# Optimization experiments

Hardware: AMD Instinct MI355X
Metric: run time of the kernel (lower is better)

The kernel has to match this reference:

```python
import jax, jax.numpy as jnp
import numpy as np

D_MODEL, N_HEADS, D_C, D_COMP, D_ROPE = 2048, 16, 512, 768, 64
D_HEAD = D_MODEL // N_HEADS  # 128
B, S = 2, 2048
ROPE_THETA = 10000.0


def _rope_cos_sin(seq_len, dim):
    # frequencies for pairwise complex rotation, dim = per-head rope dim (even)
    inv_freq = 1.0 / (ROPE_THETA ** (jnp.arange(0, dim, 2, dtype=jnp.float32) / dim))
    t = jnp.arange(seq_len, dtype=jnp.float32)
    ang = t[:, None] * inv_freq[None, :]  # [S, dim/2]
    return jnp.cos(ang), jnp.sin(ang)


def _apply_rope(x, cos, sin):
    # x: [B, S, H, dr]; rotate consecutive pairs (view_as_complex semantics)
    x1, x2 = x[..., 0::2], x[..., 1::2]
    c = cos[None, :, None, :]
    s = sin[None, :, None, :]
    y1 = x1 * c - x2 * s
    y2 = x1 * s + x2 * c
    return jnp.stack([y1, y2], axis=-1).reshape(x.shape)


def setup_inputs() -> dict:
    key = jax.random.key(0)
    ks = jax.random.split(key, 9)
    sc = 0.02
    return {
        "x": jax.random.normal(ks[0], (B, S, D_MODEL), jnp.float32),
        "Wd": jax.random.normal(ks[1], (D_MODEL, D_C), jnp.float32) * sc,
        "bd": jnp.zeros((D_C,), jnp.float32),
        "Wu": jax.random.normal(ks[2], (D_C, N_HEADS * D_HEAD), jnp.float32) * sc,
        "bu": jnp.zeros((N_HEADS * D_HEAD,), jnp.float32),
        "Wqd": jax.random.normal(ks[3], (D_MODEL, D_COMP), jnp.float32) * sc,
        "bqd": jnp.zeros((D_COMP,), jnp.float32),
        "Wqu": jax.random.normal(ks[4], (D_COMP, N_HEADS * D_HEAD), jnp.float32) * sc,
        "bqu": jnp.zeros((N_HEADS * D_HEAD,), jnp.float32),
        "Wqr": jax.random.normal(ks[5], (D_COMP, N_HEADS * D_ROPE), jnp.float32) * sc,
        "bqr": jnp.zeros((N_HEADS * D_ROPE,), jnp.float32),
        "Wkr": jax.random.normal(ks[6], (D_MODEL, N_HEADS * D_ROPE), jnp.float32) * sc,
        "bkr": jnp.zeros((N_HEADS * D_ROPE,), jnp.float32),
        "Wo": jax.random.normal(ks[7], (N_HEADS * D_HEAD, D_MODEL), jnp.float32) * sc,
        "bo": jnp.zeros((D_MODEL,), jnp.float32),
    }


def reference(x, Wd, bd, Wu, bu, Wqd, bqd, Wqu, bqu, Wqr, bqr, Wkr, bkr, Wo, bo):
    b, s, _ = x.shape
    # low-rank KV compression
    kv_c = x @ Wd + bd                                   # [B,S,d_c]
    kv_up = (kv_c @ Wu + bu).reshape(b, s, N_HEADS, D_HEAD)  # shared K-content / V
    # low-rank Q compression
    q_cmp = x @ Wqd + bqd                                # [B,S,d_comp]
    q_c = (q_cmp @ Wqu + bqu).reshape(b, s, N_HEADS, D_HEAD)
    # decoupled RoPE branches
    cos, sin = _rope_cos_sin(s, D_ROPE)
    q_r = _apply_rope((q_cmp @ Wqr + bqr).reshape(b, s, N_HEADS, D_ROPE), cos, sin)
    k_r = _apply_rope((x @ Wkr + bkr).reshape(b, s, N_HEADS, D_ROPE), cos, sin)
    q = jnp.concatenate([q_c, q_r], axis=-1)             # [B,S,H,dh+dr]
    k = jnp.concatenate([kv_up, k_r], axis=-1)           # [B,S,H,dh+dr]
    scale = 1.0 / np.sqrt(D_HEAD).astype(np.float32)
    scores = jnp.einsum('bqhd,bkhd->bhqk', q, k) * scale  # [B,H,S,S]
    probs = jax.nn.softmax(scores, axis=-1)
    out = jnp.einsum('bhqk,bkhd->bqhd', probs, kv_up)    # v == kv_up (as in source)
    out = out.reshape(b, s, N_HEADS * D_HEAD)
    return out @ Wo + bo
```

## Files before the change

kernel.cpp:

```cpp
#include <hip/hip_runtime.h>
#include <cmath>

typedef __bf16 bf16;
typedef __bf16 bf16x8 __attribute__((ext_vector_type(8)));
typedef __bf16 bf16x4 __attribute__((ext_vector_type(4)));
typedef __bf16 bf16x2 __attribute__((ext_vector_type(2)));
typedef float f32x4 __attribute__((ext_vector_type(4)));
typedef float f32x16 __attribute__((ext_vector_type(16)));
typedef int i32x4 __attribute__((ext_vector_type(4)));
typedef int i32x2 __attribute__((ext_vector_type(2)));

#define S_LEN 2048
#define QK_LD 3072

__device__ __forceinline__ void async_copy16(const bf16* g, bf16* l) {
    __builtin_amdgcn_global_load_lds(
        (const __attribute__((address_space(1))) void*)g,
        (__attribute__((address_space(3))) void*)l, 16, 0, 0);
}

__device__ __forceinline__ unsigned packbf(float a, float b) {
    bf16x2 v; v[0] = (bf16)a; v[1] = (bf16)b;
    return __builtin_bit_cast(unsigned, v);
}

__global__ __launch_bounds__(256) void cast_f32_bf16(const float* __restrict__ in,
                                                     bf16* __restrict__ out) {
    size_t i = ((size_t)blockIdx.x * 256 + threadIdx.x) * 8;
    float4 a = *(const float4*)(in + i);
    float4 b = *(const float4*)(in + i + 4);
    bf16x8 v;
    v[0] = (bf16)a.x; v[1] = (bf16)a.y; v[2] = (bf16)a.z; v[3] = (bf16)a.w;
    v[4] = (bf16)b.x; v[5] = (bf16)b.y; v[6] = (bf16)b.z; v[7] = (bf16)b.w;
    *(bf16x8*)(out + i) = v;
}

struct TSeg { const float* src; bf16* dst; int K, N, blk0; };
struct TArgs { TSeg s[7]; };

__global__ __launch_bounds__(256) void transpose_all(TArgs a) {
    __shared__ float tile[64][68];
    int b = blockIdx.x, si = 0;
#pragma unroll
    for (int i = 1; i < 7; ++i) if (b >= a.s[i].blk0) si = i;
    TSeg sg = a.s[si];
    int local = b - sg.blk0;
    int kTiles = sg.K >> 6;
    int kt = local % kTiles, nt = local / kTiles;
    int k0 = kt * 64, n0 = nt * 64;
    int K = sg.K, N = sg.N;
    int t = threadIdx.x;
#pragma unroll
    for (int i = 0; i < 4; ++i) {
        int c = t + i * 256;
        int r = c >> 4, off = (c & 15) * 4;
        float4 v = *(const float4*)(sg.src + (size_t)(k0 + r) * N + n0 + off);
        tile[r][off] = v.x; tile[r][off + 1] = v.y;
        tile[r][off + 2] = v.z; tile[r][off + 3] = v.w;
    }
    __syncthreads();
#pragma unroll
    for (int i = 0; i < 2; ++i) {
        int c = t + i * 256;
        int nr = c >> 3, koff = (c & 7) * 8;
        bf16x8 v;
#pragma unroll
        for (int j = 0; j < 8; ++j) v[j] = (bf16)tile[koff + j][nr];
        *(bf16x8*)(sg.dst + (size_t)(n0 + nr) * K + k0 + koff) = v;
    }
}

__global__ __launch_bounds__(256) void setup_small(const float* __restrict__ bd,
                                                   const float* __restrict__ bqd,
                                                   const float* __restrict__ bkr,
                                                   const float* __restrict__ bqu,
                                                   const float* __restrict__ bqr,
                                                   float* __restrict__ bcat,
                                                   float2* __restrict__ tab) {
    if (blockIdx.x < 21) {
        int i = blockIdx.x * 256 + threadIdx.x;
        if (i < 512) bcat[i] = bd[i];
        else if (i < 1280) bcat[i] = bqd[i - 512];
        else if (i < 2304) bcat[i] = bkr[i - 1280];
        else if (i < 4352) bcat[i] = bqu[i - 2304];
        else if (i < 5376) bcat[i] = bqr[i - 4352];
    } else {
        int id = (blockIdx.x - 21) * 256 + threadIdx.x;
        int s = id >> 5, i = id & 31;
        float f = expf(-0.2878231366242557f * (float)i);
        float ang = (float)s * f;
        tab[id] = make_float2(cosf(ang), sinf(ang));
    }
}

__device__ __forceinline__ void gemm_core(const bf16* __restrict__ A, int lda,
                                          const bf16* __restrict__ Bt,
                                          const float* __restrict__ bias,
                                          void* __restrict__ out0,
                                          void* __restrict__ out1,
                                          int Ndim, int Kdim, int mode,
                                          const float2* __restrict__ tab,
                                          int bn, int bm, bf16* As, bf16* Bs) {
    int t = threadIdx.x;
    int w = t >> 6, lane = t & 63;
    int wm = (w >> 1) * 64, wn = (w & 1) * 64;
    int l15 = lane & 15, q4 = lane >> 4;
    f32x4 acc[4][4] = {};

    int lrow = lane >> 2;
    int lcol = (lane & 3) * 8;
    int c0 = w * 2, c1 = w * 2 + 1;
    const bf16* aS0 = A  + (size_t)(bm * 128 + c0 * 16 + lrow) * lda + lcol;
    const bf16* aS1 = A  + (size_t)(bm * 128 + c1 * 16 + lrow) * lda + lcol;
    const bf16* bS0 = Bt + (size_t)(bn * 128 + c0 * 16 + lrow) * Kdim + lcol;
    const bf16* bS1 = Bt + (size_t)(bn * 128 + c1 * 16 + lrow) * Kdim + lcol;
    bf16* aD0 = &As[c0 * 512]; bf16* aD1 = &As[c1 * 512];
    bf16* bD0 = &Bs[c0 * 512]; bf16* bD1 = &Bs[c1 * 512];

    for (int kt = 0; kt < Kdim; kt += 32) {
        async_copy16(aS0 + kt, aD0);
        async_copy16(aS1 + kt, aD1);
        async_copy16(bS0 + kt, bD0);
        async_copy16(bS1 + kt, bD1);
        __syncthreads();
        bf16x8 af[4], bfr[4];
#pragma unroll
        for (int mb = 0; mb < 4; ++mb)
            af[mb] = *(const bf16x8*)&As[(wm + mb * 16 + l15) * 32 + q4 * 8];
#pragma unroll
        for (int nb = 0; nb < 4; ++nb)
            bfr[nb] = *(const bf16x8*)&Bs[(wn + nb * 16 + l15) * 32 + q4 * 8];
#pragma unroll
        for (int mb = 0; mb < 4; ++mb)
#pragma unroll
            for (int nb = 0; nb < 4; ++nb)
                acc[mb][nb] = __builtin_amdgcn_mfma_f32_16x16x32_bf16(
                    af[mb], bfr[nb], acc[mb][nb], 0, 0, 0);
        __syncthreads();
    }

#pragma unroll
    for (int mb = 0; mb < 4; ++mb) {
        int row = bm * 128 + wm + mb * 16 + q4 * 4;
#pragma unroll
        for (int nb = 0; nb < 4; ++nb) {
            int col = bn * 128 + wn + nb * 16 + l15;
            float bv = bias[col];
            if (mode == 1) {
#pragma unroll
                for (int r = 0; r < 4; ++r)
                    ((float*)out0)[(size_t)(row + r) * Ndim + col] = acc[mb][nb][r] + bv;
            } else if (mode == 4) {
                if (col < 1280) {
#pragma unroll
                    for (int r = 0; r < 4; ++r)
                        ((bf16*)out0)[(size_t)(row + r) * 2304 + col] =
                            (bf16)(acc[mb][nb][r] + bv);
                } else {
                    int rel = col - 1280;
                    int hh = rel >> 6, idx = rel & 63, ii = idx >> 1, odd = idx & 1;
#pragma unroll
                    for (int r = 0; r < 4; ++r) {
                        float vv = acc[mb][nb][r] + bv;
                        float pp = __shfl_xor(vv, 1, 64);
                        float2 cs = tab[((row + r) & 2047) * 32 + ii];
                        float o = vv * cs.x + (odd ? pp * cs.y : -pp * cs.y);
                        ((bf16*)out1)[(size_t)(row + r) * QK_LD + hh * 192 + 128 + idx] =
                            (bf16)o;
                    }
                }
            } else if (mode == 5) {
                if (col < 2048) {
                    int hh = col >> 7, dd = col & 127;
#pragma unroll
                    for (int r = 0; r < 4; ++r)
                        ((bf16*)out0)[(size_t)(row + r) * QK_LD + hh * 192 + dd] =
                            (bf16)(acc[mb][nb][r] + bv);
                } else {
                    int rel = col - 2048;
                    int hh = rel >> 6, idx = rel & 63, ii = idx >> 1, odd = idx & 1;
#pragma unroll
                    for (int r = 0; r < 4; ++r) {
                        float vv = acc[mb][nb][r] + bv;
                        float pp = __shfl_xor(vv, 1, 64);
                        float2 cs = tab[((row + r) & 2047) * 32 + ii];
                        float o = vv * cs.x + (odd ? pp * cs.y : -pp * cs.y);
                        ((bf16*)out0)[(size_t)(row + r) * QK_LD + hh * 192 + 128 + idx] =
                            (bf16)o;
                    }
                }
            } else {
                int hh = col >> 7, dd = col & 127;
                bf16x4 pack;
#pragma unroll
                for (int r = 0; r < 4; ++r) {
                    float vv = acc[mb][nb][r] + bv;
                    ((bf16*)out0)[(size_t)(row + r) * QK_LD + hh * 192 + dd] = (bf16)vv;
                    pack[r] = (bf16)vv;
                }
                int bidx = row >> 11, srow = row & 2047;
                *(bf16x4*)((bf16*)out1 +
                           ((size_t)(bidx * 16 + hh) * 128 + dd) * S_LEN + srow) = pack;
            }
        }
    }
}

__global__ __launch_bounds__(256) void gemm_bt(const bf16* __restrict__ A, int lda,
                                               const bf16* __restrict__ Bt,
                                               const float* __restrict__ bias,
                                               void* __restrict__ out0,
                                               void* __restrict__ out1,
                                               int Ndim, int Kdim, int mode,
                                               const float2* __restrict__ tab) {
    __shared__ bf16 As[128 * 32];
    __shared__ bf16 Bs[128 * 32];
    gemm_core(A, lda, Bt, bias, out0, out1, Ndim, Kdim, mode, tab,
              blockIdx.x, blockIdx.y, As, Bs);
}

__global__ __launch_bounds__(256) void gemm_up(const bf16* __restrict__ xproj,
                                               const bf16* __restrict__ WuT,
                                               const float* __restrict__ bu,
                                               void* __restrict__ kbuf,
                                               void* __restrict__ vt,
                                               const bf16* __restrict__ W2T,
                                               const float* __restrict__ bq,
                                               void* __restrict__ qbuf,
                                               const float2* __restrict__ tab) {
    __shared__ bf16 As[128 * 32];
    __shared__ bf16 Bs[128 * 32];
    int bn = blockIdx.x;
    if (bn < 16)
        gemm_core(xproj, 2304, WuT, bu, kbuf, vt, 2048, 512, 6, tab,
                  bn, blockIdx.y, As, Bs);
    else
        gemm_core(xproj + 512, 2304, W2T, bq, qbuf, nullptr, 3072, 768, 5, tab,
                  bn - 16, blockIdx.y, As, Bs);
}

__global__ __launch_bounds__(512, 2) void attn(const bf16* __restrict__ qbuf,
                                               const bf16* __restrict__ kbuf,
                                               const bf16* __restrict__ vt,
                                               bf16* __restrict__ attnout) {
    __shared__ bf16 Ks[2][32 * 192];
    __shared__ bf16 Vs[2][128 * 32];
    int bh = blockIdx.x;
    int qt = blockIdx.y;
    int b = bh >> 4, h = bh & 15;
    int t = threadIdx.x, w = t >> 6, lane = t & 63;
    int l31 = lane & 31, hl = lane >> 5;
    const float scale = 0.08838834764831845f;

    bf16x8 qf[12];
    {
        size_t rbase = (size_t)(b * S_LEN + qt * 256 + w * 32 + l31) * QK_LD
                       + h * 192 + hl * 8;
#pragma unroll
        for (int c = 0; c < 12; ++c)
            qf[c] = *(const bf16x8*)(qbuf + rbase + c * 16);
    }

    f32x16 oacc[4] = {};
    float denom = 0.f;
    const bf16* kb_base = kbuf + (size_t)b * S_LEN * QK_LD + h * 192;
    const bf16* vt_base = vt + (size_t)bh * 128 * S_LEN;

    int kg0, klA0, klB0, kg1, klA1, klB1, vg0, vlA0, vlB0;
    {
        int c = t;
        int kr = c / 24, u = c % 24;
        kg0 = kr * QK_LD + u * 8;
        int m = kr & 15;
        klA0 = kr * 192 + (((2 * u) ^ m) << 2);
        klB0 = kr * 192 + (((2 * u + 1) ^ m) << 2);
    }
    {
        int c = t + 512;
        int kr = c / 24, u = c % 24;
        kg1 = kr * QK_LD + u * 8;
        int m = kr & 15;
        klA1 = kr * 192 + (((2 * u) ^ m) << 2);
        klB1 = kr * 192 + (((2 * u + 1) ^ m) << 2);
    }
    {
        int c = t;
        int vd = c >> 2, u = c & 3;
        vg0 = vd * S_LEN + u * 8;
        int line = vd >> 1, lm = line & 15;
        int sl = 8 * (vd & 1) + 2 * u;
        vlA0 = line * 64 + ((sl ^ lm) << 2);
        vlB0 = line * 64 + (((sl + 1) ^ lm) << 2);
    }
    bool kx = (t < 256);

    int mK = l31 & 15;
    int kRow = l31 * 192;
    int vLM = l31 >> 1;
    int vSlotB = 8 * (l31 & 1) + 2 * hl;

    i32x4 kreg0, kreg1, vreg0;
    kreg0 = *(const i32x4*)(kb_base + kg0);
    if (kx) kreg1 = *(const i32x4*)(kb_base + kg1);
    vreg0 = *(const i32x4*)(vt_base + vg0);
    {
        i32x2 lo; lo[0] = kreg0[0]; lo[1] = kreg0[1];
        i32x2 hi; hi[0] = kreg0[2]; hi[1] = kreg0[3];
        *(i32x2*)&Ks[0][klA0] = lo;
        *(i32x2*)&Ks[0][klB0] = hi;
        if (kx) {
            i32x2 lo1; lo1[0] = kreg1[0]; lo1[1] = kreg1[1];
            i32x2 hi1; hi1[0] = kreg1[2]; hi1[1] = kreg1[3];
            *(i32x2*)&Ks[0][klA1] = lo1;
            *(i32x2*)&Ks[0][klB1] = hi1;
        }
        i32x2 lov; lov[0] = vreg0[0]; lov[1] = vreg0[1];
        i32x2 hiv; hiv[0] = vreg0[2]; hiv[1] = vreg0[3];
        *(i32x2*)&Vs[0][vlA0] = lov;
        *(i32x2*)&Vs[0][vlB0] = hiv;
    }
    __syncthreads();

    int cur = 0;
    for (int kt = 0; kt < 64; ++kt) {
        if (kt < 63) {
            const bf16* kb = kb_base + (size_t)(kt + 1) * 32 * QK_LD;
            kreg0 = *(const i32x4*)(kb + kg0);
            if (kx) kreg1 = *(const i32x4*)(kb + kg1);
            vreg0 = *(const i32x4*)(vt_base + (kt + 1) * 32 + vg0);
        }

        f32x16 sacc = {};
        __builtin_amdgcn_s_setprio(1);
#pragma unroll
        for (int c = 0; c < 12; ++c) {
            int u0 = 4 * c + 2 * hl;
            i32x2 lo = *(const i32x2*)&Ks[cur][kRow + ((u0 ^ mK) << 2)];
            i32x2 hi = *(const i32x2*)&Ks[cur][kRow + (((u0 + 1) ^ mK) << 2)];
            i32x4 kv; kv[0] = lo[0]; kv[1] = lo[1]; kv[2] = hi[0]; kv[3] = hi[1];
            bf16x8 kb = __builtin_bit_cast(bf16x8, kv);
            sacc = __builtin_amdgcn_mfma_f32_32x32x16_bf16(kb, qf[c], sacc, 0, 0, 0);
        }
        __builtin_amdgcn_s_setprio(0);

        unsigned W[8], pw[8];
#pragma unroll
        for (int m = 0; m < 8; ++m) {
            float e0 = __expf(fminf(sacc[2 * m] * scale, 50.0f));
            float e1 = __expf(fminf(sacc[2 * m + 1] * scale, 50.0f));
            denom += e0 + e1;
            W[m] = packbf(e0, e1);
        }
#pragma unroll
        for (int m = 0; m < 8; ++m)
            pw[m] = (unsigned)__shfl_xor((int)W[m], 32, 64);
        bf16x8 paf[2];
#pragma unroll
        for (int s = 0; s < 2; ++s) {
            unsigned A = hl ? pw[4 * s + 2] : W[4 * s + 0];
            unsigned B = hl ? pw[4 * s + 3] : W[4 * s + 1];
            unsigned C = hl ? W[4 * s + 2] : pw[4 * s + 0];
            unsigned D = hl ? W[4 * s + 3] : pw[4 * s + 1];
            i32x4 di; di[0] = (int)A; di[1] = (int)B; di[2] = (int)C; di[3] = (int)D;
            paf[s] = __builtin_bit_cast(bf16x8, di);
        }

        __builtin_amdgcn_s_setprio(1);
#pragma unroll
        for (int dg = 0; dg < 4; ++dg) {
#pragma unroll
            for (int s = 0; s < 2; ++s) {
                int line = dg * 16 + (l31 >> 1);
                int s0 = (vSlotB + 4 * s) ^ vLM;
                int s1 = (vSlotB + 4 * s + 1) ^ vLM;
                i32x2 lo = *(const i32x2*)&Vs[cur][line * 64 + (s0 << 2)];
                i32x2 hi = *(const i32x2*)&Vs[cur][line * 64 + (s1 << 2)];
                i32x4 vv; vv[0] = lo[0]; vv[1] = lo[1]; vv[2] = hi[0]; vv[3] = hi[1];
                bf16x8 vb = __builtin_bit_cast(bf16x8, vv);
                oacc[dg] = __builtin_amdgcn_mfma_f32_32x32x16_bf16(
                    paf[s], vb, oacc[dg], 0, 0, 0);
            }
        }
        __builtin_amdgcn_s_setprio(0);

        if (kt < 63) {
            i32x2 lo; lo[0] = kreg0[0]; lo[1] = kreg0[1];
            i32x2 hi; hi[0] = kreg0[2]; hi[1] = kreg0[3];
            *(i32x2*)&Ks[cur ^ 1][klA0] = lo;
            *(i32x2*)&Ks[cur ^ 1][klB0] = hi;
            if (kx) {
                i32x2 lo1; lo1[0] = kreg1[0]; lo1[1] = kreg1[1];
                i32x2 hi1; hi1[0] = kreg1[2]; hi1[1] = kreg1[3];
                *(i32x2*)&Ks[cur ^ 1][klA1] = lo1;
                *(i32x2*)&Ks[cur ^ 1][klB1] = hi1;
            }
            i32x2 lov; lov[0] = vreg0[0]; lov[1] = vreg0[1];
            i32x2 hiv; hiv[0] = vreg0[2]; hiv[1] = vreg0[3];
            *(i32x2*)&Vs[cur ^ 1][vlA0] = lov;
            *(i32x2*)&Vs[cur ^ 1][vlB0] = hiv;
        }
        __syncthreads();
        cur ^= 1;
    }

    denom += __shfl_xor(denom, 32, 64);

#pragma unroll
    for (int r = 0; r < 16; ++r) {
        int rowl = (r & 3) + 8 * (r >> 2) + 4 * hl;
        float dv = __shfl(denom, rowl, 64);
        float inv = 1.0f / dv;
        int row = qt * 256 + w * 32 + rowl;
#pragma unroll
        for (int dg = 0; dg < 4; ++dg) {
            int col = h * 128 + dg * 32 + l31;
            attnout[(size_t)(b * S_LEN + row) * 2048 + col] =
                (bf16)(oacc[dg][r] * inv);
        }
    }
}

extern "C" void kernel_launch(void* const* d_in, const int* in_sizes, int n_in,
                              void* d_out, int out_size, void* d_ws, size_t ws_size,
                              hipStream_t stream) {
    const float* x   = (const float*)d_in[0];
    const float* Wd  = (const float*)d_in[1];
    const float* bd  = (const float*)d_in[2];
    const float* Wu  = (const float*)d_in[3];
    const float* bu  = (const float*)d_in[4];
    const float* Wqd = (const float*)d_in[5];
    const float* bqd = (const float*)d_in[6];
    const float* Wqu = (const float*)d_in[7];
    const float* bqu = (const float*)d_in[8];
    const float* Wqr = (const float*)d_in[9];
    const float* bqr = (const float*)d_in[10];
    const float* Wkr = (const float*)d_in[11];
    const float* bkr = (const float*)d_in[12];
    const float* Wo  = (const float*)d_in[13];
    const float* bo  = (const float*)d_in[14];
    float* out = (float*)d_out;

    char* p = (char*)d_ws;
    auto alloc = [&](size_t n) { char* r = p; p += (n + 255) & ~(size_t)255; return r; };
    bf16* xb    = (bf16*)alloc((size_t)4096 * 2048 * 2);
    bf16* W1T   = (bf16*)alloc((size_t)2304 * 2048 * 2);
    bf16* W2T   = (bf16*)alloc((size_t)3072 * 768 * 2);
    bf16* WuT   = (bf16*)alloc((size_t)2048 * 512 * 2);
    bf16* WoT   = (bf16*)alloc((size_t)2048 * 2048 * 2);
    bf16* xproj = (bf16*)alloc((size_t)4096 * 2304 * 2);
    bf16* qbuf  = (bf16*)alloc((size_t)4096 * 3072 * 2);
    bf16* kbuf  = (bf16*)alloc((size_t)4096 * 3072 * 2);
    bf16* vt    = (bf16*)alloc((size_t)32 * 128 * 2048 * 2);
    bf16* aout  = (bf16*)alloc((size_t)4096 * 2048 * 2);
    float* bcat = (float*)alloc((size_t)5376 * 4);
    float2* tab = (float2*)alloc((size_t)65536 * 8);

    cast_f32_bf16<<<dim3(4096), dim3(256), 0, stream>>>(x, xb);

    TArgs ta;
    ta.s[0] = {Wd,  W1T,                       2048, 512,  0};
    ta.s[1] = {Wqd, W1T + (size_t)512 * 2048,  2048, 768,  256};
    ta.s[2] = {Wkr, W1T + (size_t)1280 * 2048, 2048, 1024, 640};
    ta.s[3] = {Wqu, W2T,                       768,  2048, 1152};
    ta.s[4] = {Wqr, W2T + (size_t)2048 * 768,  768,  1024, 1536};
    ta.s[5] = {Wu,  WuT,                       512,  2048, 1728};
    ta.s[6] = {Wo,  WoT,                       2048, 2048, 1984};
    transpose_all<<<dim3(3008), dim3(256), 0, stream>>>(ta);
    setup_small<<<dim3(277), dim3(256), 0, stream>>>(bd, bqd, bkr, bqu, bqr, bcat, tab);

    gemm_bt<<<dim3(18, 32), dim3(256), 0, stream>>>(xb, 2048, W1T, bcat,
                                                    xproj, kbuf, 2304, 2048, 4, tab);
    gemm_up<<<dim3(40, 32), dim3(256), 0, stream>>>(xproj, WuT, bu, kbuf, vt,
                                                    W2T, bcat + 2304, qbuf, tab);

    attn<<<dim3(32, 8), dim3(512), 0, stream>>>(qbuf, kbuf, vt, aout);

    gemm_bt<<<dim3(16, 32), dim3(256), 0, stream>>>(aout, 2048, WoT, bo,
                                                    out, nullptr, 2048, 2048, 1, tab);
}
```

Baseline: 430.2 us.

## Triple-buffer GEMM LDS tiles with two-stage async prefetch

```diff
diff --git a/kernel.cpp b/kernel.cpp
--- a/kernel.cpp
+++ b/kernel.cpp
@@ -117,26 +117,53 @@
     bf16* aD0 = &As[c0 * 512]; bf16* aD1 = &As[c1 * 512];
     bf16* bD0 = &Bs[c0 * 512]; bf16* bD1 = &Bs[c1 * 512];
 
-    for (int kt = 0; kt < Kdim; kt += 32) {
-        async_copy16(aS0 + kt, aD0);
-        async_copy16(aS1 + kt, aD1);
-        async_copy16(bS0 + kt, bD0);
-        async_copy16(bS1 + kt, bD1);
-        __syncthreads();
+    int nk = Kdim >> 5;
+
+    async_copy16(aS0, aD0);
+    async_copy16(aS1, aD1);
+    async_copy16(bS0, bD0);
+    async_copy16(bS1, bD1);
+    async_copy16(aS0 + 32, aD0 + 4096);
+    async_copy16(aS1 + 32, aD1 + 4096);
+    async_copy16(bS0 + 32, bD0 + 4096);
+    async_copy16(bS1 + 32, bD1 + 4096);
+    asm volatile("s_waitcnt vmcnt(4)" ::: "memory");
+    __builtin_amdgcn_s_barrier();
+    __builtin_amdgcn_sched_barrier(0);
+
+    int cur = 0;
+    for (int ti = 0; ti < nk; ++ti) {
+        if (ti + 2 < nk) {
+            int sb = cur + 2; if (sb >= 3) sb -= 3;
+            int ko = (ti + 2) << 5;
+            async_copy16(aS0 + ko, aD0 + sb * 4096);
+            async_copy16(aS1 + ko, aD1 + sb * 4096);
+            async_copy16(bS0 + ko, bD0 + sb * 4096);
+            async_copy16(bS1 + ko, bD1 + sb * 4096);
+        }
+        const bf16* Ab = As + cur * 4096;
+        const bf16* Bb = Bs + cur * 4096;
         bf16x8 af[4], bfr[4];
 #pragma unroll
         for (int mb = 0; mb < 4; ++mb)
-            af[mb] = *(const bf16x8*)&As[(wm + mb * 16 + l15) * 32 + q4 * 8];
+            af[mb] = *(const bf16x8*)&Ab[(wm + mb * 16 + l15) * 32 + q4 * 8];
 #pragma unroll
         for (int nb = 0; nb < 4; ++nb)
-            bfr[nb] = *(const bf16x8*)&Bs[(wn + nb * 16 + l15) * 32 + q4 * 8];
+            bfr[nb] = *(const bf16x8*)&Bb[(wn + nb * 16 + l15) * 32 + q4 * 8];
 #pragma unroll
         for (int mb = 0; mb < 4; ++mb)
 #pragma unroll
             for (int nb = 0; nb < 4; ++nb)
                 acc[mb][nb] = __builtin_amdgcn_mfma_f32_16x16x32_bf16(
                     af[mb], bfr[nb], acc[mb][nb], 0, 0, 0);
-        __syncthreads();
+        __builtin_amdgcn_sched_barrier(0);
+        if (ti + 2 < nk)
+            asm volatile("s_waitcnt vmcnt(4)" ::: "memory");
+        else
+            asm volatile("s_waitcnt vmcnt(0)" ::: "memory");
+        __builtin_amdgcn_s_barrier();
+        __builtin_amdgcn_sched_barrier(0);
+        cur = (cur == 2) ? 0 : cur + 1;
     }
 
 #pragma unroll
@@ -213,8 +240,8 @@
                                                void* __restrict__ out1,
                                                int Ndim, int Kdim, int mode,
                                                const float2* __restrict__ tab) {
-    __shared__ bf16 As[128 * 32];
-    __shared__ bf16 Bs[128 * 32];
+    __shared__ bf16 As[3 * 128 * 32];
+    __shared__ bf16 Bs[3 * 128 * 32];
     gemm_core(A, lda, Bt, bias, out0, out1, Ndim, Kdim, mode, tab,
               blockIdx.x, blockIdx.y, As, Bs);
 }
@@ -228,8 +255,8 @@
                                                const float* __restrict__ bq,
                                                void* __restrict__ qbuf,
                                                const float2* __restrict__ tab) {
-    __shared__ bf16 As[128 * 32];
-    __shared__ bf16 Bs[128 * 32];
+    __shared__ bf16 As[3 * 128 * 32];
+    __shared__ bf16 Bs[3 * 128 * 32];
     int bn = blockIdx.x;
     if (bn < 16)
         gemm_core(xproj, 2304, WuT, bu, kbuf, vt, 2048, 512, 6, tab,
```

After: 432.1 us. Within noise of the previous version (+0.5%).

## Split GEMM K dimension across two warp groups with LDS reduction

Applied to the files above, without the earlier changes.

```diff
diff --git a/kernel.cpp b/kernel.cpp
--- a/kernel.cpp
+++ b/kernel.cpp
@@ -102,22 +102,27 @@
                                           const float2* __restrict__ tab,
                                           int bn, int bm, bf16* As, bf16* Bs) {
     int t = threadIdx.x;
-    int w = t >> 6, lane = t & 63;
+    int kg = t >> 8;
+    int t2 = t & 255;
+    int w = t2 >> 6, lane = t2 & 63;
     int wm = (w >> 1) * 64, wn = (w & 1) * 64;
     int l15 = lane & 15, q4 = lane >> 4;
     f32x4 acc[4][4] = {};
 
+    int kh = Kdim >> 1;
     int lrow = lane >> 2;
     int lcol = (lane & 3) * 8;
     int c0 = w * 2, c1 = w * 2 + 1;
-    const bf16* aS0 = A  + (size_t)(bm * 128 + c0 * 16 + lrow) * lda + lcol;
-    const bf16* aS1 = A  + (size_t)(bm * 128 + c1 * 16 + lrow) * lda + lcol;
-    const bf16* bS0 = Bt + (size_t)(bn * 128 + c0 * 16 + lrow) * Kdim + lcol;
-    const bf16* bS1 = Bt + (size_t)(bn * 128 + c1 * 16 + lrow) * Kdim + lcol;
-    bf16* aD0 = &As[c0 * 512]; bf16* aD1 = &As[c1 * 512];
-    bf16* bD0 = &Bs[c0 * 512]; bf16* bD1 = &Bs[c1 * 512];
-
-    for (int kt = 0; kt < Kdim; kt += 32) {
+    const bf16* aS0 = A  + (size_t)(bm * 128 + c0 * 16 + lrow) * lda + lcol + kg * kh;
+    const bf16* aS1 = A  + (size_t)(bm * 128 + c1 * 16 + lrow) * lda + lcol + kg * kh;
+    const bf16* bS0 = Bt + (size_t)(bn * 128 + c0 * 16 + lrow) * Kdim + lcol + kg * kh;
+    const bf16* bS1 = Bt + (size_t)(bn * 128 + c1 * 16 + lrow) * Kdim + lcol + kg * kh;
+    bf16* Asg = As + kg * 4096;
+    bf16* Bsg = Bs + kg * 4096;
+    bf16* aD0 = &Asg[c0 * 512]; bf16* aD1 = &Asg[c1 * 512];
+    bf16* bD0 = &Bsg[c0 * 512]; bf16* bD1 = &Bsg[c1 * 512];
+
+    for (int kt = 0; kt < kh; kt += 32) {
         async_copy16(aS0 + kt, aD0);
         async_copy16(aS1 + kt, aD1);
         async_copy16(bS0 + kt, bD0);
@@ -126,10 +131,10 @@
         bf16x8 af[4], bfr[4];
 #pragma unroll
         for (int mb = 0; mb < 4; ++mb)
-            af[mb] = *(const bf16x8*)&As[(wm + mb * 16 + l15) * 32 + q4 * 8];
+            af[mb] = *(const bf16x8*)&Asg[(wm + mb * 16 + l15) * 32 + q4 * 8];
 #pragma unroll
         for (int nb = 0; nb < 4; ++nb)
-            bfr[nb] = *(const bf16x8*)&Bs[(wn + nb * 16 + l15) * 32 + q4 * 8];
+            bfr[nb] = *(const bf16x8*)&Bsg[(wn + nb * 16 + l15) * 32 + q4 * 8];
 #pragma unroll
         for (int mb = 0; mb < 4; ++mb)
 #pragma unroll
@@ -138,6 +143,24 @@
                     af[mb], bfr[nb], acc[mb][nb], 0, 0, 0);
         __syncthreads();
     }
+
+    float* red = (float*)As;
+#pragma unroll
+    for (int mb2 = 0; mb2 < 4; ++mb2) {
+        if (kg == 1) {
+#pragma unroll
+            for (int nb = 0; nb < 4; ++nb)
+                *(f32x4*)&red[t2 * 16 + nb * 4] = acc[mb2][nb];
+        }
+        __syncthreads();
+        if (kg == 0) {
+#pragma unroll
+            for (int nb = 0; nb < 4; ++nb)
+                acc[mb2][nb] += *(const f32x4*)&red[t2 * 16 + nb * 4];
+        }
+        __syncthreads();
+    }
+    if (kg == 1) return;
 
 #pragma unroll
     for (int mb = 0; mb < 4; ++mb) {
@@ -206,30 +229,30 @@
     }
 }
 
-__global__ __launch_bounds__(256) void gemm_bt(const bf16* __restrict__ A, int lda,
-                                               const bf16* __restrict__ Bt,
-                                               const float* __restrict__ bias,
-                                               void* __restrict__ out0,
-                                               void* __restrict__ out1,
-                                               int Ndim, int Kdim, int mode,
-                                               const float2* __restrict__ tab) {
-    __shared__ bf16 As[128 * 32];
-    __shared__ bf16 Bs[128 * 32];
+__global__ __launch_bounds__(512, 4) void gemm_bt(const bf16* __restrict__ A, int lda,
+                                                  const bf16* __restrict__ Bt,
+                                                  const float* __restrict__ bias,
+                                                  void* __restrict__ out0,
+                                                  void* __restrict__ out1,
+                                                  int Ndim, int Kdim, int mode,
+                                                  const float2* __restrict__ tab) {
+    __shared__ bf16 As[2 * 128 * 32];
+    __shared__ bf16 Bs[2 * 128 * 32];
     gemm_core(A, lda, Bt, bias, out0, out1, Ndim, Kdim, mode, tab,
               blockIdx.x, blockIdx.y, As, Bs);
 }
 
-__global__ __launch_bounds__(256) void gemm_up(const bf16* __restrict__ xproj,
-                                               const bf16* __restrict__ WuT,
-                                               const float* __restrict__ bu,
-                                               void* __restrict__ kbuf,
-                                               void* __restrict__ vt,
-                                               const bf16* __restrict__ W2T,
-                                               const float* __restrict__ bq,
-                                               void* __restrict__ qbuf,
-                                               const float2* __restrict__ tab) {
-    __shared__ bf16 As[128 * 32];
-    __shared__ bf16 Bs[128 * 32];
+__global__ __launch_bounds__(512, 4) void gemm_up(const bf16* __restrict__ xproj,
+                                                  const bf16* __restrict__ WuT,
+                                                  const float* __restrict__ bu,
+                                                  void* __restrict__ kbuf,
+                                                  void* __restrict__ vt,
+                                                  const bf16* __restrict__ W2T,
+                                                  const float* __restrict__ bq,
+                                                  void* __restrict__ qbuf,
+                                                  const float2* __restrict__ tab) {
+    __shared__ bf16 As[2 * 128 * 32];
+    __shared__ bf16 Bs[2 * 128 * 32];
     int bn = blockIdx.x;
     if (bn < 16)
         gemm_core(xproj, 2304, WuT, bu, kbuf, vt, 2048, 512, 6, tab,
@@ -468,13 +491,13 @@
     transpose_all<<<dim3(3008), dim3(256), 0, stream>>>(ta);
     setup_small<<<dim3(277), dim3(256), 0, stream>>>(bd, bqd, bkr, bqu, bqr, bcat, tab);
 
-    gemm_bt<<<dim3(18, 32), dim3(256), 0, stream>>>(xb, 2048, W1T, bcat,
+    gemm_bt<<<dim3(18, 32), dim3(512), 0, stream>>>(xb, 2048, W1T, bcat,
                                                     xproj, kbuf, 2304, 2048, 4, tab);
-    gemm_up<<<dim3(40, 32), dim3(256), 0, stream>>>(xproj, WuT, bu, kbuf, vt,
+    gemm_up<<<dim3(40, 32), dim3(512), 0, stream>>>(xproj, WuT, bu, kbuf, vt,
                                                     W2T, bcat + 2304, qbuf, tab);
 
     attn<<<dim3(32, 8), dim3(512), 0, stream>>>(qbuf, kbuf, vt, aout);
 
-    gemm_bt<<<dim3(16, 32), dim3(256), 0, stream>>>(aout, 2048, WoT, bo,
+    gemm_bt<<<dim3(16, 32), dim3(512), 0, stream>>>(aout, 2048, WoT, bo,
                                                     out, nullptr, 2048, 2048, 1, tab);
 }
```

Result: no change. 432.4 us (+0.5%).
